# Kernel tuning notes

Measured on AMD Instinct MI355X. Metric: run time of the kernel, lower is better.

The kernel has to match this reference:

```python
import jax, jax.numpy as jnp
import numpy as np

INPUT_DIM = 1024
NUM_OUTPUTS = 1024
BIT_SIZE = 256


def setup_inputs() -> dict:
    key = jax.random.key(0)
    k1, k2 = jax.random.split(key)
    # x: binary input bits, shape (input_dim, bit_size)
    x = jax.random.randint(k1, (INPUT_DIM, BIT_SIZE), 0, 2).astype(jnp.int32)
    # kernel: per-(input, output) Bernoulli probabilities in [0, 1)
    kernel = jax.random.uniform(k2, (INPUT_DIM, NUM_OUTPUTS), dtype=jnp.float32)
    return {"x": x, "kernel": kernel}


def reference(x, kernel):
    # Sample per-weight Bernoulli bit vectors: w[i, n, b] ~ Bernoulli(kernel[i, n])
    # (fused equivalent of the original nested-loop np.random.binomial calls)
    rng = jax.random.key(42)
    u = jax.random.uniform(rng, kernel.shape + (BIT_SIZE,), dtype=kernel.dtype)
    w = u < kernel[:, :, None]  # bool (input_dim, num_outputs, bit_size)

    # Original loop: temp = (x & w[:, n]).sum(axis=0); y[n] = (temp > 0)
    # == OR-reduction over input_dim of the bitwise AND.
    xb = x.astype(bool)  # (input_dim, bit_size)
    y = jnp.any(xb[:, None, :] & w, axis=0)  # (num_outputs, bit_size)
    return y.astype(jnp.float32)
```

## Files before the change

### kernel.cpp

```cpp
#include <hip/hip_runtime.h>


#define INPUT_DIM 1024
#define NUM_OUTPUTS 1024
#define BIT_SIZE 256

__device__ __forceinline__ uint32_t rotl32(uint32_t v, int r) {
    return (v << r) | (v >> (32 - r));
}

__device__ __forceinline__ void threefry2x32(uint32_t k0, uint32_t k1,
                                             uint32_t& x0, uint32_t& x1) {
    const uint32_t ks0 = k0;
    const uint32_t ks1 = k1;
    const uint32_t ks2 = k0 ^ k1 ^ 0x1BD11BDAu;
    x0 += ks0;
    x1 += ks1;
#define TF_ROUND(r) { x0 += x1; x1 = rotl32(x1, (r)); x1 ^= x0; }
    TF_ROUND(13) TF_ROUND(15) TF_ROUND(26) TF_ROUND(6)
    x0 += ks1; x1 += ks2 + 1u;
    TF_ROUND(17) TF_ROUND(29) TF_ROUND(16) TF_ROUND(24)
    x0 += ks2; x1 += ks0 + 2u;
    TF_ROUND(13) TF_ROUND(15) TF_ROUND(26) TF_ROUND(6)
    x0 += ks0; x1 += ks1 + 3u;
    TF_ROUND(17) TF_ROUND(29) TF_ROUND(16) TF_ROUND(24)
    x0 += ks1; x1 += ks2 + 4u;
    TF_ROUND(13) TF_ROUND(15) TF_ROUND(26) TF_ROUND(6)
    x0 += ks2; x1 += ks0 + 5u;
#undef TF_ROUND
}

__global__ __launch_bounds__(256) void pack_x_kernel(const int* __restrict__ x,
                                                     uint32_t* __restrict__ xm) {
    const int b = threadIdx.x;
    const int w = blockIdx.x;
    uint32_t m = 0;
#pragma unroll
    for (int j = 0; j < 32; ++j) {
        m |= (x[(((w << 5) + j) << 8) + b] != 0 ? 1u : 0u) << j;
    }
    xm[(w << 8) + b] = m;
}

__global__ __launch_bounds__(256) void BitLayer_25391846654323_kernel(
        const uint32_t* __restrict__ xm,
        const float* __restrict__ kern,
        float* __restrict__ out) {
    const int b = blockIdx.x >> 2;
    const int n = ((blockIdx.x & 3) << 8) + threadIdx.x;
    uint32_t done = 0;

    for (int w = 0; w < 32; ++w) {
        uint32_t m = xm[(w << 8) + b];
        while (m) {
            const int j = __builtin_ctz(m);
            m &= m - 1;
            const int i = (w << 5) + j;
            const float p = kern[(i << 10) + n];
            if (!done) {
                uint32_t c0 = (((uint32_t)(i & 511)) << 18) |
                              ((uint32_t)n << 8) | (uint32_t)b;
                uint32_t c1 = c0 + (1u << 27);
                threefry2x32(0u, 42u, c0, c1);
                const uint32_t bits = (i < 512) ? c0 : c1;
                const float u = (float)(bits >> 9) * 0x1p-23f;
                if (u < p) done = 1u;
            }
            if (__all(done != 0)) goto finished;
        }
    }
finished:
    out[((uint32_t)n << 8) + (uint32_t)b] = done ? 1.0f : 0.0f;
}

extern "C" void kernel_launch(void* const* d_in, const int* in_sizes, int n_in,
                              void* d_out, int out_size, void* d_ws, size_t ws_size,
                              hipStream_t stream) {
    const int* x = (const int*)d_in[0];
    const float* kern = (const float*)d_in[1];
    float* out = (float*)d_out;
    uint32_t* xm = (uint32_t*)d_ws;

    pack_x_kernel<<<32, 256, 0, stream>>>(x, xm);
    BitLayer_25391846654323_kernel<<<NUM_OUTPUTS, 256, 0, stream>>>(xm, kern, out);
}
```

Baseline: 64.70 us.

## Batch eight active inputs per iteration and preload transposed bit masks

The packed x masks are stored transposed so each block loads its 32 mask words contiguously into registers up front. The inner loop now pulls up to eight set bits at a time, issues their eight kernel-probability loads together, then runs eight independent threefry evaluations before the wave-wide early-exit check. This exposes memory-level and instruction-level parallelism and checks the early exit less often. In exchange it can do up to seven wasted RNG evaluations per batch once lanes finish, including duplicate evaluations when fewer than eight bits remain, and it raises register pressure.

```diff
diff --git a/kernel.cpp b/kernel.cpp
--- a/kernel.cpp
+++ b/kernel.cpp
@@ -31,7 +31,7 @@
 }
 
 __global__ __launch_bounds__(256) void pack_x_kernel(const int* __restrict__ x,
-                                                     uint32_t* __restrict__ xm) {
+                                                     uint32_t* __restrict__ xmT) {
     const int b = threadIdx.x;
     const int w = blockIdx.x;
     uint32_t m = 0;
@@ -39,32 +39,45 @@
     for (int j = 0; j < 32; ++j) {
         m |= (x[(((w << 5) + j) << 8) + b] != 0 ? 1u : 0u) << j;
     }
-    xm[(w << 8) + b] = m;
+    xmT[(b << 5) + w] = m;
 }
 
 __global__ __launch_bounds__(256) void BitLayer_25391846654323_kernel(
-        const uint32_t* __restrict__ xm,
+        const uint32_t* __restrict__ xmT,
         const float* __restrict__ kern,
         float* __restrict__ out) {
     const int b = blockIdx.x >> 2;
     const int n = ((blockIdx.x & 3) << 8) + threadIdx.x;
+    const uint32_t nb = ((uint32_t)n << 8) | (uint32_t)b;
+
+    uint32_t mask[32];
+#pragma unroll
+    for (int w = 0; w < 32; ++w) mask[w] = xmT[(b << 5) + w];
+
     uint32_t done = 0;
-
     for (int w = 0; w < 32; ++w) {
-        uint32_t m = xm[(w << 8) + b];
+        uint32_t m = mask[w];
         while (m) {
-            const int j = __builtin_ctz(m);
+            const int i0 = (w << 5) + __builtin_ctz(m);
             m &= m - 1;
-            const int i = (w << 5) + j;
-            const float p = kern[(i << 10) + n];
-            if (!done) {
-                uint32_t c0 = (((uint32_t)(i & 511)) << 18) |
-                              ((uint32_t)n << 8) | (uint32_t)b;
+            int ii[8];
+            ii[0] = i0;
+#pragma unroll
+            for (int k = 1; k < 8; ++k) {
+                if (m) { ii[k] = (w << 5) + __builtin_ctz(m); m &= m - 1; }
+                else   { ii[k] = i0; }
+            }
+            float p[8];
+#pragma unroll
+            for (int k = 0; k < 8; ++k) p[k] = kern[(ii[k] << 10) + n];
+#pragma unroll
+            for (int k = 0; k < 8; ++k) {
+                uint32_t c0 = (((uint32_t)(ii[k] & 511)) << 18) | nb;
                 uint32_t c1 = c0 + (1u << 27);
                 threefry2x32(0u, 42u, c0, c1);
-                const uint32_t bits = (i < 512) ? c0 : c1;
+                const uint32_t bits = (ii[k] < 512) ? c0 : c1;
                 const float u = (float)(bits >> 9) * 0x1p-23f;
-                if (u < p) done = 1u;
+                if (u < p[k]) done = 1u;
             }
             if (__all(done != 0)) goto finished;
         }
@@ -79,8 +92,8 @@
     const int* x = (const int*)d_in[0];
     const float* kern = (const float*)d_in[1];
     float* out = (float*)d_out;
-    uint32_t* xm = (uint32_t*)d_ws;
+    uint32_t* xmT = (uint32_t*)d_ws;
 
-    pack_x_kernel<<<32, 256, 0, stream>>>(x, xm);
-    BitLayer_25391846654323_kernel<<<NUM_OUTPUTS, 256, 0, stream>>>(xm, kern, out);
+    pack_x_kernel<<<32, 256, 0, stream>>>(x, xmT);
+    BitLayer_25391846654323_kernel<<<NUM_OUTPUTS, 256, 0, stream>>>(xmT, kern, out);
 }
```

Result: slower. 66.95 us (+3.5%).
